# Kernel optimization log

Hardware: AMD Instinct MI355X
Metric: run time of the kernel (lower is better)

The kernel has to match this reference:

```python
import jax, jax.numpy as jnp
import numpy as np

PH = PW = 8
HEADS = 8
ADIM = 256
DH = ADIM // HEADS
N_KEYS = 3
CK, CV, CQ = 16, 32, 16
KS = 7
K_PDIM = PH * PW * CK   # 1024
V_PDIM = PH * PW * CV   # 2048
Q_PDIM = PH * PW * CQ   # 1024
MB_IN = N_KEYS * CV     # 96
MB_HID = 4 * MB_IN      # 384


def _to_patches(x):
    # b c (h ph) (w pw) -> b (h w) (ph pw c)
    b, c, H, W = x.shape
    h, w = H // PH, W // PW
    x = x.reshape(b, c, h, PH, w, PW).transpose(0, 2, 4, 3, 5, 1)
    return x.reshape(b, h * w, PH * PW * c)


def _layernorm(x, g, b):
    m = x.mean(-1, keepdims=True)
    v = x.var(-1, keepdims=True)
    return (x - m) * jax.lax.rsqrt(v + 1e-5) * g + b


def _embed(x, W1, b1, W2, b2):
    # NonLinearEmbedding: Linear -> GELU -> Linear
    return jax.nn.gelu(x @ W1 + b1) @ W2 + b2


def _to_heads(x):
    # b n (h d) -> b h n d
    b, n, hd = x.shape
    return x.reshape(b, n, HEADS, hd // HEADS).transpose(0, 2, 1, 3)


def _conv(x, w, b, groups, pad):
    y = jax.lax.conv_general_dilated(
        x, w, (1, 1), pad,
        dimension_numbers=('NCHW', 'OIHW', 'NCHW'),
        feature_group_count=groups)
    return y + b[None, :, None, None]


def _mbconv(x, w_exp, b_exp, w_dw, b_dw, w_proj, b_proj):
    # grouped 1x1 expand -> GELU -> depthwise kxk -> GELU -> grouped 1x1 project
    h = jax.nn.gelu(_conv(x, w_exp, b_exp, HEADS, 'VALID'))
    h = jax.nn.gelu(_conv(h, w_dw, b_dw, MB_HID, 'SAME'))
    return _conv(h, w_proj, b_proj, HEADS, 'VALID')


def setup_inputs() -> dict:
    key = jax.random.key(0)
    ks = jax.random.split(key, 24)
    B = 2
    key_sizes = [(256, 256), (192, 320), (128, 128)]
    query_sizes = [(256, 256), (192, 192)]
    s = 0.02
    inp = {}
    for i, (h, w) in enumerate(key_sizes):
        inp[f'keys_{i}'] = jax.random.normal(ks[i], (B, CK, h, w), jnp.float32)
        inp[f'values_{i}'] = jax.random.normal(ks[3 + i], (B, CV, h, w), jnp.float32)
    for i, (h, w) in enumerate(query_sizes):
        inp[f'queries_{i}'] = jax.random.normal(ks[6 + i], (B, CQ, h, w), jnp.float32)
    inp['ln_g'] = jnp.ones((V_PDIM,), jnp.float32)
    inp['ln_b'] = jnp.zeros((V_PDIM,), jnp.float32)
    inp['kW1'] = jax.random.normal(ks[8], (K_PDIM, ADIM), jnp.float32) * s
    inp['kb1'] = jnp.zeros((ADIM,), jnp.float32)
    inp['kW2'] = jax.random.normal(ks[9], (ADIM, ADIM), jnp.float32) * s
    inp['kb2'] = jnp.zeros((ADIM,), jnp.float32)
    inp['qW1'] = jax.random.normal(ks[10], (Q_PDIM, ADIM), jnp.float32) * s
    inp['qb1'] = jnp.zeros((ADIM,), jnp.float32)
    inp['qW2'] = jax.random.normal(ks[11], (ADIM, ADIM), jnp.float32) * s
    inp['qb2'] = jnp.zeros((ADIM,), jnp.float32)
    inp['w_exp'] = jax.random.normal(ks[12], (MB_HID, MB_IN // HEADS, 1, 1), jnp.float32) * s
    inp['b_exp'] = jnp.zeros((MB_HID,), jnp.float32)
    inp['w_dw'] = jax.random.normal(ks[13], (MB_HID, 1, KS, KS), jnp.float32) * s
    inp['b_dw'] = jnp.zeros((MB_HID,), jnp.float32)
    inp['w_proj'] = jax.random.normal(ks[14], (CV, MB_HID // HEADS, 1, 1), jnp.float32) * s
    inp['b_proj'] = jnp.zeros((CV,), jnp.float32)
    return inp


def reference(keys_0, keys_1, keys_2, values_0, values_1, values_2,
              queries_0, queries_1, ln_g, ln_b, kW1, kb1, kW2, kb2,
              qW1, qb1, qW2, qb2, w_exp, b_exp, w_dw, b_dw, w_proj, b_proj):
    keys = [keys_0, keys_1, keys_2]
    values = [values_0, values_1, values_2]
    queries = [queries_0, queries_1]
    # spatial sizes are already multiples of (PH, PW) -> pad_to_next_multiple is identity
    query_sizes = [q.shape[-2:] for q in queries]
    kp = [_to_patches(k) for k in keys]
    vp = [_to_patches(v) for v in values]
    qp = [_to_patches(q) for q in queries]
    nk = [p.shape[1] for p in kp]
    nq = [p.shape[1] for p in qp]
    k_seq = jnp.concatenate(kp, axis=1)               # (b, Nk, K_PDIM)
    v_seq = _layernorm(jnp.concatenate(vp, axis=1), ln_g, ln_b)  # (b, Nk, V_PDIM)
    q_seq = jnp.concatenate(qp, axis=1)               # (b, Nq, Q_PDIM)
    k_emb = _to_heads(_embed(k_seq, kW1, kb1, kW2, kb2))  # (b, h, Nk, DH)
    q_emb = _to_heads(_embed(q_seq, qW1, qb1, qW2, qb2))  # (b, h, Nq, DH)
    v_h = _to_heads(v_seq)                                # (b, h, Nk, dv)
    scale = jnp.asarray(1.0 / np.sqrt(DH), k_emb.dtype)
    attn = jnp.einsum('bhid,bhjd->bhij', q_emb, k_emb) * scale
    attn = jax.nn.softmax(attn, axis=-1)
    offs = np.cumsum([0] + nk)
    # per-source weighted values, stacked along a new source axis k
    weighted = jnp.stack(
        [attn[..., offs[i]:offs[i + 1]] @ v_h[:, :, offs[i]:offs[i + 1]]
         for i in range(N_KEYS)], axis=1)              # (b, k, h, Nq, dv)
    qoffs = np.cumsum([0] + nq)
    outs = []
    c = CV // HEADS
    for i, (qh, qw) in enumerate(query_sizes):
        v = weighted[:, :, :, qoffs[i]:qoffs[i + 1]]   # (b, k, hd, n, d)
        b, k, hd, n, d = v.shape
        h, w = qh // PH, qw // PW
        # b k hd (h w) (ph pw c) -> b (hd k c) (h ph) (w pw)
        v = v.reshape(b, k, hd, h, w, PH, PW, c).transpose(0, 2, 1, 7, 3, 5, 4, 6)
        v = v.reshape(b, hd * k * c, h * PH, w * PW)
        outs.append(_mbconv(v, w_exp, b_exp, w_dw, b_dw, w_proj, b_proj))
    return tuple(outs)
```

## Files before the change

kernel.cpp:

```cpp
#include <hip/hip_runtime.h>
#include <hip/hip_bf16.h>
#include <math.h>

typedef unsigned short bfu;
typedef __attribute__((ext_vector_type(8))) short short8v;
typedef __attribute__((ext_vector_type(4))) float f32x4;
typedef __attribute__((ext_vector_type(2))) float f32x2;

__device__ __forceinline__ float fast_rcp(float d) {
    float r = __builtin_amdgcn_rcpf(d);
    return r * fmaf(-d, r, 2.0f);
}
__device__ __forceinline__ f32x2 fma2(f32x2 a, f32x2 b, f32x2 c) {
    return __builtin_elementwise_fma(a, b, c);
}
__device__ __forceinline__ f32x2 splat2(float w) { return (f32x2){w, w}; }
__device__ __forceinline__ float gelu_f(float x) {
    float x3 = x * x * x;
    float e = __expf(1.5957691f * fmaf(0.044715f, x3, x));
    return x * e * __builtin_amdgcn_rcpf(e + 1.0f);
}
__device__ __forceinline__ f32x2 gelu2(f32x2 x) {
    f32x2 x3 = x * x * x;
    f32x2 z = fma2(splat2(0.044715f), x3, x) * 1.5957691f;
    f32x2 e = {__expf(z.x), __expf(z.y)};
    f32x2 d = e + 1.0f;
    f32x2 r = {__builtin_amdgcn_rcpf(d.x), __builtin_amdgcn_rcpf(d.y)};
    return x * e * r;
}
__device__ __forceinline__ float bf2f(bfu u) {
    union { float f; unsigned int i; } v; v.i = ((unsigned int)u) << 16; return v.f;
}
__device__ __forceinline__ bfu f2bf(float f) {
    union { float f; unsigned int i; } v; v.f = f;
    unsigned int r = v.i + 0x7fff + ((v.i >> 16) & 1);
    return (bfu)(r >> 16);
}
__device__ __forceinline__ float ldin(const void* p, size_t i, bool f32) {
    return f32 ? ((const float*)p)[i] : bf2f(((const bfu*)p)[i]);
}
__device__ __forceinline__ void stout(void* p, size_t i, float v, bool f32) {
    if (f32) ((float*)p)[i] = v;
    else     ((bfu*)p)[i] = f2bf(v);
}
__device__ __forceinline__ short8v ld_frag8(const bfu* p) {
    union { short8v v; ushort4 u[2]; } t;
    t.u[0] = *(const ushort4*)p;
    t.u[1] = *(const ushort4*)(p + 4);
    return t.v;
}

__global__ __launch_bounds__(256) void detect_kernel(const void* probe, int* flag) {
    __shared__ int red[4];
    const bfu* p = (const bfu*)probe;
    int tid = threadIdx.x;
    int insane = 0;
    for (int i = tid; i < 2048; i += 256) {
        unsigned e = (p[i] >> 7) & 0xFF;
        if (e >= 0xC0 || (e != 0 && e < 0x40)) insane++;
    }
    for (int o = 32; o > 0; o >>= 1) insane += __shfl_down(insane, o);
    if ((tid & 63) == 0) red[tid >> 6] = insane;
    __syncthreads();
    if (tid == 0) flag[0] = (red[0] + red[1] + red[2] + red[3] > 64) ? 1 : 0;
}

__global__ __launch_bounds__(256) void zero_out_kernel(bfu* __restrict__ out, int n) {
    int i = blockIdx.x * 256 + threadIdx.x;
    if (i < n) out[i] = 0;
}

__global__ __launch_bounds__(256) void wprep_kernel(
    const void* __restrict__ wexp, const void* __restrict__ bexp,
    const void* __restrict__ wdw, const void* __restrict__ bdw,
    const void* __restrict__ wproj, const void* __restrict__ bproj,
    const int* __restrict__ flag, float* __restrict__ wf)
{
    bool f32 = flag[0] != 0;
    int i = blockIdx.x * 256 + threadIdx.x;
    if (i < 4608)       wf[i] = ldin(wexp, i, f32);
    else if (i < 4992)  wf[i] = ldin(bexp, i - 4608, f32);
    else if (i < 23808) wf[i] = ldin(wdw, i - 4992, f32);
    else if (i < 24192) wf[i] = ldin(bdw, i - 23808, f32);
    else if (i < 25728) wf[i] = ldin(wproj, i - 24192, f32);
    else if (i < 25760) wf[i] = ldin(bproj, i - 25728, f32);
}

__global__ __launch_bounds__(256) void ln_stats_kernel(
    const void* __restrict__ v0, const void* __restrict__ v1, const void* __restrict__ v2,
    const int* __restrict__ flag, float* __restrict__ m_buf, float* __restrict__ i_buf)
{
    __shared__ float red[16];
    bool f32 = flag[0] != 0;
    int bid = blockIdx.x;
    int b = bid / 2240, n = bid - b * 2240;
    const void* src; int nl, wp, H, W;
    if (n < 1024)      { src = v0; nl = n;        wp = 32; H = 256; W = 256; }
    else if (n < 1984) { src = v1; nl = n - 1024; wp = 40; H = 192; W = 320; }
    else               { src = v2; nl = n - 1984; wp = 16; H = 128; W = 128; }
    int tid = threadIdx.x;
    int py = nl / wp, px = nl - py * wp;
    int ybase = py * 8, xbase = px * 8;
    float s1 = 0.f, s2 = 0.f;
    #pragma unroll
    for (int i = 0; i < 8; i++) {
        int j = tid + 256 * i;
        int ph = j >> 8, pw = (j >> 5) & 7, c = j & 31;
        float v = ldin(src, ((size_t)(b * 32 + c) * H + ybase + ph) * W + xbase + pw, f32);
        s1 += v; s2 = fmaf(v, v, s2);
    }
    for (int o = 32; o > 0; o >>= 1) { s1 += __shfl_down(s1, o); s2 += __shfl_down(s2, o); }
    int wid = tid >> 6;
    if ((tid & 63) == 0) { red[wid] = s1; red[8 + wid] = s2; }
    __syncthreads();
    if (tid == 0) {
        float a = red[0] + red[1] + red[2] + red[3];
        float q = red[8] + red[9] + red[10] + red[11];
        float m = a * (1.0f / 2048.0f);
        float var = q * (1.0f / 2048.0f) - m * m;
        m_buf[bid] = m;
        i_buf[bid] = 1.0f / sqrtf(var + 1e-5f);
    }
}

__global__ __launch_bounds__(256) void vstage_kernel(
    const void* __restrict__ v0, const void* __restrict__ v1, const void* __restrict__ v2,
    const void* __restrict__ g, const void* __restrict__ beta,
    const int* __restrict__ flag, bfu* __restrict__ out)
{
    __shared__ float red[16];
    __shared__ float mv[2];
    bool f32 = flag[0] != 0;
    int bid = blockIdx.x;
    int b = bid / 2240, n = bid - b * 2240;
    const void* src; int nl, wp, H, W;
    if (n < 1024)      { src = v0; nl = n;        wp = 32; H = 256; W = 256; }
    else if (n < 1984) { src = v1; nl = n - 1024; wp = 40; H = 192; W = 320; }
    else               { src = v2; nl = n - 1984; wp = 16; H = 128; W = 128; }
    int tid = threadIdx.x;
    int py = nl / wp, px = nl - py * wp;
    int ybase = py * 8, xbase = px * 8;
    float vals[8];
    float s1 = 0.f, s2 = 0.f;
    #pragma unroll
    for (int i = 0; i < 8; i++) {
        int j = tid + 256 * i;
        int ph = j >> 8, pw = (j >> 5) & 7, c = j & 31;
        float v = ldin(src, ((size_t)(b * 32 + c) * H + ybase + ph) * W + xbase + pw, f32);
        vals[i] = v; s1 += v; s2 = fmaf(v, v, s2);
    }
    for (int o = 32; o > 0; o >>= 1) { s1 += __shfl_down(s1, o); s2 += __shfl_down(s2, o); }
    int wid = tid >> 6;
    if ((tid & 63) == 0) { red[wid] = s1; red[8 + wid] = s2; }
    __syncthreads();
    if (tid == 0) {
        float a = red[0] + red[1] + red[2] + red[3];
        float q = red[8] + red[9] + red[10] + red[11];
        float m = a * (1.0f / 2048.0f);
        float var = q * (1.0f / 2048.0f) - m * m;
        mv[0] = m; mv[1] = 1.0f / sqrtf(var + 1e-5f);
    }
    __syncthreads();
    float m = mv[0], inv = mv[1];
    #pragma unroll
    for (int i = 0; i < 8; i++) {
        int j = tid + 256 * i;
        float o = (vals[i] - m) * inv * ldin(g, j, f32) + ldin(beta, j, f32);
        out[(size_t)bid * 2048 + j] = f2bf(o);
    }
}

__global__ __launch_bounds__(256) void vtr_kernel(
    const bfu* __restrict__ vseq, bfu* __restrict__ vT)
{
    __shared__ __align__(16) bfu Ls[17408];
    int bid = blockIdx.x;
    int ch = bid % 35;
    int t = bid / 35;
    int h = t & 7, b = t >> 3;
    int c = threadIdx.x;
    const bfu* srcb = vseq + (((size_t)(b * 2240 + (ch << 6))) << 11) + (h << 8) + c;
    #pragma unroll
    for (int k4 = 0; k4 < 16; k4++) {
        ushort4 v;
        v.x = srcb[(size_t)(k4 * 4 + 0) << 11];
        v.y = srcb[(size_t)(k4 * 4 + 1) << 11];
        v.z = srcb[(size_t)(k4 * 4 + 2) << 11];
        v.w = srcb[(size_t)(k4 * 4 + 3) << 11];
        *(ushort4*)&Ls[c * 68 + k4 * 4] = v;
    }
    __syncthreads();
    short8v* dst = (short8v*)(vT + (size_t)((b * 8 + h) * 35 + ch) * 17408);
    const short8v* s = (const short8v*)Ls;
    #pragma unroll
    for (int r = 0; r < 8; r++) dst[(r << 8) + c] = s[(r << 8) + c];
    if (c < 128) dst[2048 + c] = s[2048 + c];
}

__global__ __launch_bounds__(256) void embed1_kernel(
    const void* __restrict__ k0, const void* __restrict__ k1, const void* __restrict__ k2,
    const void* __restrict__ q0, const void* __restrict__ q1,
    const void* __restrict__ kW1, const void* __restrict__ kb1,
    const void* __restrict__ qW1, const void* __restrict__ qb1,
    const int* __restrict__ flag,
    bfu* __restrict__ k_hid, bfu* __restrict__ q_hid)
{
    __shared__ float As[16][68];
    __shared__ float Bs[16][68];
    bool f32 = flag[0] != 0;
    int bid = blockIdx.x;
    int colBase = (bid & 3) << 6;
    int rt = bid >> 2;
    const void* Wm; const void* bias; bfu* C;
    int rowBase, isK;
    if (rt < 70) { isK = 1; Wm = kW1; bias = kb1; C = k_hid; rowBase = rt << 6; }
    else         { isK = 0; Wm = qW1; bias = qb1; C = q_hid; rowBase = (rt - 70) << 6; }
    int tid = threadIdx.x;
    int tx = tid & 15, ty = tid >> 4;
    int arow = tid >> 2, akq = (tid & 3) << 2;
    int brow = tid >> 4, bcol = (tid & 15) << 2;
    int row = rowBase + arow;
    int nTot = isK ? 2240 : 1600;
    int b = row / nTot, n = row - b * nTot;
    const void* src; int nl, wp, H, W;
    if (isK) {
        if (n < 1024)      { src = k0; nl = n;        wp = 32; H = 256; W = 256; }
        else if (n < 1984) { src = k1; nl = n - 1024; wp = 40; H = 192; W = 320; }
        else               { src = k2; nl = n - 1984; wp = 16; H = 128; W = 128; }
    } else {
        if (n < 1024)      { src = q0; nl = n;        wp = 32; H = 256; W = 256; }
        else               { src = q1; nl = n - 1024; wp = 24; H = 192; W = 192; }
    }
    int py = nl / wp, px = nl - py * wp;
    int ybase = py << 3, xbase = px << 3;
    size_t HW = (size_t)H * W;
    size_t abase = (size_t)(b * 16 + akq) * HW;
    size_t wbase = (size_t)brow * 256 + colBase + bcol;
    float acc[4][4] = {};
    for (int k0i = 0; k0i < 1024; k0i += 16) {
        int j = k0i + akq;
        int ph = j >> 7, pw = (j >> 4) & 7;
        size_t ai = abase + (size_t)(ybase + ph) * W + xbase + pw;
        As[akq + 0][arow] = ldin(src, ai, f32);
        As[akq + 1][arow] = ldin(src, ai + HW, f32);
        As[akq + 2][arow] = ldin(src, ai + 2 * HW, f32);
        As[akq + 3][arow] = ldin(src, ai + 3 * HW, f32);
        size_t wo = wbase + (size_t)k0i * 256;
        #pragma unroll
        for (int t = 0; t < 4; t++) Bs[brow][bcol + t] = ldin(Wm, wo + t, f32);
        __syncthreads();
        #pragma unroll
        for (int kk = 0; kk < 16; kk++) {
            float4 a4 = *(const float4*)&As[kk][ty << 2];
            float4 p0 = *(const float4*)&Bs[kk][tx << 2];
            float ar[4] = {a4.x, a4.y, a4.z, a4.w};
            float br[4] = {p0.x, p0.y, p0.z, p0.w};
            #pragma unroll
            for (int rr = 0; rr < 4; rr++)
                #pragma unroll
                for (int i = 0; i < 4; i++)
                    acc[rr][i] = fmaf(ar[rr], br[i], acc[rr][i]);
        }
        __syncthreads();
    }
    int cg = colBase + (tx << 2);
    float bbr[4];
    #pragma unroll
    for (int i = 0; i < 4; i++) bbr[i] = ldin(bias, cg + i, f32);
    #pragma unroll
    for (int rr = 0; rr < 4; rr++) {
        ushort4 o;
        o.x = f2bf(gelu_f(acc[rr][0] + bbr[0]));
        o.y = f2bf(gelu_f(acc[rr][1] + bbr[1]));
        o.z = f2bf(gelu_f(acc[rr][2] + bbr[2]));
        o.w = f2bf(gelu_f(acc[rr][3] + bbr[3]));
        *(ushort4*)(&C[(size_t)(rowBase + (ty << 2) + rr) * 256 + cg]) = o;
    }
}

__global__ __launch_bounds__(256) void embed2_kernel(
    const bfu* __restrict__ A0, const void* __restrict__ W0, const void* __restrict__ bias0,
    bfu* __restrict__ C0, int tiles0,
    const bfu* __restrict__ A1, const void* __restrict__ W1, const void* __restrict__ bias1,
    bfu* __restrict__ C1, const int* __restrict__ flag)
{
    __shared__ float As[16][68];
    __shared__ float Bs[16][68];
    bool f32 = flag[0] != 0;
    int bid = blockIdx.x;
    int colBase = (bid & 3) << 6;
    int rt = bid >> 2;
    const bfu* A; const void* Wm; const void* bias; bfu* C;
    int rowBase;
    if (rt < tiles0) { A = A0; Wm = W0; bias = bias0; C = C0; rowBase = rt << 6; }
    else             { A = A1; Wm = W1; bias = bias1; C = C1; rowBase = (rt - tiles0) << 6; }
    int tid = threadIdx.x;
    int tx = tid & 15, ty = tid >> 4;
    int arow = tid >> 2, akq = (tid & 3) << 2;
    int brow = tid >> 4, bcol = (tid & 15) << 2;
    const bfu* Ap = A + (size_t)(rowBase + arow) * 256 + akq;
    size_t wbase = (size_t)brow * 256 + colBase + bcol;
    float acc[4][4] = {};
    for (int k0 = 0; k0 < 256; k0 += 16) {
        ushort4 av = *(const ushort4*)(Ap + k0);
        As[akq + 0][arow] = bf2f(av.x);
        As[akq + 1][arow] = bf2f(av.y);
        As[akq + 2][arow] = bf2f(av.z);
        As[akq + 3][arow] = bf2f(av.w);
        size_t wo = wbase + (size_t)k0 * 256;
        #pragma unroll
        for (int t = 0; t < 4; t++) Bs[brow][bcol + t] = ldin(Wm, wo + t, f32);
        __syncthreads();
        #pragma unroll
        for (int kk = 0; kk < 16; kk++) {
            float4 a4 = *(const float4*)&As[kk][ty << 2];
            float4 p0 = *(const float4*)&Bs[kk][tx << 2];
            float ar[4] = {a4.x, a4.y, a4.z, a4.w};
            float br[4] = {p0.x, p0.y, p0.z, p0.w};
            #pragma unroll
            for (int rr = 0; rr < 4; rr++)
                #pragma unroll
                for (int i = 0; i < 4; i++)
                    acc[rr][i] = fmaf(ar[rr], br[i], acc[rr][i]);
        }
        __syncthreads();
    }
    int cg = colBase + (tx << 2);
    float bbr[4];
    #pragma unroll
    for (int i = 0; i < 4; i++) bbr[i] = ldin(bias, cg + i, f32);
    #pragma unroll
    for (int rr = 0; rr < 4; rr++) {
        ushort4 o;
        o.x = f2bf(acc[rr][0] + bbr[0]);
        o.y = f2bf(acc[rr][1] + bbr[1]);
        o.z = f2bf(acc[rr][2] + bbr[2]);
        o.w = f2bf(acc[rr][3] + bbr[3]);
        *(ushort4*)(&C[(size_t)(rowBase + (ty << 2) + rr) * 256 + cg]) = o;
    }
}

__global__ __launch_bounds__(256) void attn_mfma_kernel(
    const bfu* __restrict__ qe, const bfu* __restrict__ ke,
    const bfu* __restrict__ vT,
    bfu* __restrict__ wbuf, float* __restrict__ lbuf, int h0, int hs)
{
    __shared__ __align__(16) bfu Vs[17408];
    __shared__ __align__(16) bfu Ps[2176];
    __shared__ float red[4][16];
    int bid = blockIdx.x;
    int qtile = bid % 50;
    int t = bid / 50;
    int hh = t % hs, b = t / hs;
    int h = h0 + hh;
    int n0 = qtile << 5;
    int tid = threadIdx.x;
    int w = tid >> 6, l = tid & 63;
    int l15 = l & 15, g = l >> 4;
    int wqt = w >> 1;
    int wkp = (w & 1) << 1;

    short8v qf = *(const short8v*)(qe + (((size_t)(b * 1600 + n0 + (wqt << 4) + l15)) << 8) + (h << 5) + (g << 3));

    f32x4 zero4 = {0.f, 0.f, 0.f, 0.f};
    f32x4 acc[2][4];
    #pragma unroll
    for (int i = 0; i < 2; i++)
        #pragma unroll
        for (int j = 0; j < 4; j++) acc[i][j] = zero4;
    float rs = 0.f;
    const float scale = 0.17677669529663687f;

    const short8v* vbase = (const short8v*)(vT + (size_t)((b * 8 + h) * 35) * 17408);
    short8v* VsV = (short8v*)Vs;

    for (int ch = 0; ch < 35; ch++) {
        const short8v* src = vbase + (size_t)ch * 2176;
        #pragma unroll
        for (int r = 0; r < 8; r++) VsV[(r << 8) + tid] = src[(r << 8) + tid];
        if (tid < 128) VsV[2048 + tid] = src[2048 + tid];
        #pragma unroll
        for (int j = 0; j < 2; j++) {
            int ktile = wkp + j;
            short8v kf = *(const short8v*)(ke + (((size_t)(b * 2240 + (ch << 6) + (ktile << 4) + l15)) << 8) + (h << 5) + (g << 3));
            f32x4 st = __builtin_amdgcn_mfma_f32_16x16x32_bf16(kf, qf, zero4, 0, 0, 0);
            float p0 = __expf(st[0] * scale);
            float p1 = __expf(st[1] * scale);
            float p2 = __expf(st[2] * scale);
            float p3 = __expf(st[3] * scale);
            rs += (p0 + p1) + (p2 + p3);
            ushort4 pk;
            pk.x = f2bf(p0); pk.y = f2bf(p1); pk.z = f2bf(p2); pk.w = f2bf(p3);
            *(ushort4*)&Ps[((wqt << 4) + l15) * 68 + (ktile << 4) + (g << 2)] = pk;
        }
        __syncthreads();
        #pragma unroll
        for (int kt = 0; kt < 2; kt++) {
            short8v a0 = ld_frag8(&Ps[l15 * 68 + (kt << 5) + (g << 3)]);
            short8v a1 = ld_frag8(&Ps[(16 + l15) * 68 + (kt << 5) + (g << 3)]);
            #pragma unroll
            for (int nt = 0; nt < 4; nt++) {
                int ntg = (w << 2) + nt;
                short8v bf = ld_frag8(&Vs[((ntg << 4) + l15) * 68 + (kt << 5) + (g << 3)]);
                acc[0][nt] = __builtin_amdgcn_mfma_f32_16x16x32_bf16(a0, bf, acc[0][nt], 0, 0, 0);
                acc[1][nt] = __builtin_amdgcn_mfma_f32_16x16x32_bf16(a1, bf, acc[1][nt], 0, 0, 0);
            }
        }
        __syncthreads();
        if (ch == 15 || ch == 30 || ch == 34) {
            int srcid = (ch == 15) ? 0 : (ch == 30 ? 1 : 2);
            bfu* wb = wbuf + ((size_t)((b * hs + hh) * 3 + srcid) * 1600 + n0) * 256 + (w << 6) + l15;
            #pragma unroll
            for (int q2 = 0; q2 < 2; q2++)
                #pragma unroll
                for (int nt = 0; nt < 4; nt++) {
                    #pragma unroll
                    for (int r = 0; r < 4; r++) {
                        wb[(size_t)((q2 << 4) + (g << 2) + r) * 256 + (nt << 4)] = f2bf(acc[q2][nt][r]);
                        acc[q2][nt][r] = 0.f;
                    }
                }
        }
    }
    rs += __shfl_xor(rs, 16);
    rs += __shfl_xor(rs, 32);
    if (l < 16) red[w][l15] = rs;
    __syncthreads();
    if (tid < 32) {
        int q2 = tid >> 4;
        float tot = red[q2 << 1][tid & 15] + red[(q2 << 1) + 1][tid & 15];
        lbuf[(size_t)(b * 8 + h) * 1600 + n0 + tid] = tot;
    }
}

__global__ __launch_bounds__(256) void attn_kernel(
    const bfu* __restrict__ qe, const bfu* __restrict__ ke,
    const bfu* __restrict__ vseq,
    const void* __restrict__ v0, const void* __restrict__ v1, const void* __restrict__ v2,
    const void* __restrict__ ln_g, const void* __restrict__ ln_b,
    const float* __restrict__ m_buf, const float* __restrict__ i_buf,
    const int* __restrict__ flag,
    bfu* __restrict__ wbuf, float* __restrict__ lbuf, int h0, int hs)
{
    __shared__ float Qs[32][36];
    __shared__ float Ks[32][37];
    __shared__ float Ps2[32][37];
    __shared__ float Vls[32][260];
    __shared__ float gbg[256];
    __shared__ float gbb[256];
    bool f32 = flag[0] != 0;
    int bid = blockIdx.x;
    int qt = bid % 50;
    int t = bid / 50;
    int hh = t % hs;
    int b = t / hs;
    int h = h0 + hh;
    int n0 = qt << 5;
    int tid = threadIdx.x;
    int tx = tid & 15, ty = tid >> 4;
    if (!vseq) {
        gbg[tid] = ldin(ln_g, h * 256 + tid, f32);
        gbb[tid] = ldin(ln_b, h * 256 + tid, f32);
    }
    {
        int r = tid >> 3, d0 = (tid & 7) << 2;
        const bfu* qp = qe + (size_t)(b * 1600 + n0 + r) * 256 + (h << 5) + d0;
        ushort4 a = *(const ushort4*)qp;
        Qs[r][d0 + 0] = bf2f(a.x); Qs[r][d0 + 1] = bf2f(a.y);
        Qs[r][d0 + 2] = bf2f(a.z); Qs[r][d0 + 3] = bf2f(a.w);
    }
    float lreg = 0.f;
    float acc[2][4][4] = {};
    const float scale = 0.17677669529663687f;
    int kvrow = tid >> 3, kq = (tid & 7) << 2;
    const bfu* kbase = ke + (size_t)(b * 2240 + kvrow) * 256 + (h << 5) + kq;
    const bfu* vsbase = vseq ? vseq + (size_t)(b * 2240 + kvrow) * 2048 + (h << 8) + kq : nullptr;
    for (int ch = 0; ch < 70; ch++) {
        {
            ushort4 kv = *(const ushort4*)(kbase + (size_t)ch * 8192);
            Ks[kvrow][kq + 0] = bf2f(kv.x);
            Ks[kvrow][kq + 1] = bf2f(kv.y);
            Ks[kvrow][kq + 2] = bf2f(kv.z);
            Ks[kvrow][kq + 3] = bf2f(kv.w);
        }
        if (vseq) {
            #pragma unroll
            for (int i = 0; i < 8; i++) {
                ushort4 u = *(const ushort4*)(vsbase + (size_t)ch * 65536 + (i << 5));
                int d = (i << 5) + kq;
                Vls[kvrow][d + 0] = bf2f(u.x);
                Vls[kvrow][d + 1] = bf2f(u.y);
                Vls[kvrow][d + 2] = bf2f(u.z);
                Vls[kvrow][d + 3] = bf2f(u.w);
            }
        } else {
            int n = ch * 32 + kvrow;
            const void* vsrc; int nl, wp, H, W;
            if (n < 1024)      { vsrc = v0; nl = n;        wp = 32; H = 256; W = 256; }
            else if (n < 1984) { vsrc = v1; nl = n - 1024; wp = 40; H = 192; W = 320; }
            else               { vsrc = v2; nl = n - 1984; wp = 16; H = 128; W = 128; }
            int py = nl / wp, px = nl - py * wp;
            int y = py * 8 + h, xb = px * 8;
            float m = m_buf[b * 2240 + n];
            float inv = i_buf[b * 2240 + n];
            size_t HW = (size_t)H * W;
            size_t vbi = ((size_t)(b * 32 + kq) * H + y) * W + xb;
            #pragma unroll
            for (int i = 0; i < 8; i++) {
                int d = (i << 5) + kq;
                float t0 = (ldin(vsrc, vbi + i, f32) - m) * inv;
                float t1 = (ldin(vsrc, vbi + i + HW, f32) - m) * inv;
                float t2 = (ldin(vsrc, vbi + i + 2 * HW, f32) - m) * inv;
                float t3 = (ldin(vsrc, vbi + i + 3 * HW, f32) - m) * inv;
                Vls[kvrow][d + 0] = fmaf(t0, gbg[d + 0], gbb[d + 0]);
                Vls[kvrow][d + 1] = fmaf(t1, gbg[d + 1], gbb[d + 1]);
                Vls[kvrow][d + 2] = fmaf(t2, gbg[d + 2], gbb[d + 2]);
                Vls[kvrow][d + 3] = fmaf(t3, gbg[d + 3], gbb[d + 3]);
            }
        }
        __syncthreads();
        float s[2][2] = {};
        #pragma unroll 8
        for (int d = 0; d < 32; d++) {
            float k0v = Ks[(tx << 1) + 0][d];
            float k1v = Ks[(tx << 1) + 1][d];
            #pragma unroll
            for (int rr = 0; rr < 2; rr++) {
                float qv = Qs[(ty << 1) + rr][d];
                s[rr][0] = fmaf(qv, k0v, s[rr][0]);
                s[rr][1] = fmaf(qv, k1v, s[rr][1]);
            }
        }
        #pragma unroll
        for (int rr = 0; rr < 2; rr++) {
            Ps2[(ty << 1) + rr][(tx << 1) + 0] = __expf(s[rr][0] * scale);
            Ps2[(ty << 1) + rr][(tx << 1) + 1] = __expf(s[rr][1] * scale);
        }
        __syncthreads();
        if (tid < 32) {
            float t2 = 0.f;
            #pragma unroll
            for (int jj = 0; jj < 32; jj++) t2 += Ps2[tid][jj];
            lreg += t2;
        }
        #pragma unroll 4
        for (int j = 0; j < 32; j++) {
            float4 w0 = *(const float4*)&Vls[j][(tx << 2)];
            float4 w1 = *(const float4*)&Vls[j][64 + (tx << 2)];
            float4 w2 = *(const float4*)&Vls[j][128 + (tx << 2)];
            float4 w3 = *(const float4*)&Vls[j][192 + (tx << 2)];
            #pragma unroll
            for (int rr = 0; rr < 2; rr++) {
                float p = Ps2[(ty << 1) + rr][j];
                acc[rr][0][0] = fmaf(p, w0.x, acc[rr][0][0]);
                acc[rr][0][1] = fmaf(p, w0.y, acc[rr][0][1]);
                acc[rr][0][2] = fmaf(p, w0.z, acc[rr][0][2]);
                acc[rr][0][3] = fmaf(p, w0.w, acc[rr][0][3]);
                acc[rr][1][0] = fmaf(p, w1.x, acc[rr][1][0]);
                acc[rr][1][1] = fmaf(p, w1.y, acc[rr][1][1]);
                acc[rr][1][2] = fmaf(p, w1.z, acc[rr][1][2]);
                acc[rr][1][3] = fmaf(p, w1.w, acc[rr][1][3]);
                acc[rr][2][0] = fmaf(p, w2.x, acc[rr][2][0]);
                acc[rr][2][1] = fmaf(p, w2.y, acc[rr][2][1]);
                acc[rr][2][2] = fmaf(p, w2.z, acc[rr][2][2]);
                acc[rr][2][3] = fmaf(p, w2.w, acc[rr][2][3]);
                acc[rr][3][0] = fmaf(p, w3.x, acc[rr][3][0]);
                acc[rr][3][1] = fmaf(p, w3.y, acc[rr][3][1]);
                acc[rr][3][2] = fmaf(p, w3.z, acc[rr][3][2]);
                acc[rr][3][3] = fmaf(p, w3.w, acc[rr][3][3]);
            }
        }
        __syncthreads();
        if (ch == 31 || ch == 61 || ch == 69) {
            int src = (ch == 31) ? 0 : (ch == 61 ? 1 : 2);
            bfu* wb = wbuf + (size_t)(((b * hs + hh) * 3 + src) * 1600 + n0 + (ty << 1)) * 256 + (tx << 2);
            #pragma unroll
            for (int rr = 0; rr < 2; rr++) {
                #pragma unroll
                for (int q = 0; q < 4; q++) {
                    ushort4 u;
                    u.x = f2bf(acc[rr][q][0]); u.y = f2bf(acc[rr][q][1]);
                    u.z = f2bf(acc[rr][q][2]); u.w = f2bf(acc[rr][q][3]);
                    *(ushort4*)(wb + (size_t)rr * 256 + (q << 6)) = u;
                    acc[rr][q][0] = acc[rr][q][1] = acc[rr][q][2] = acc[rr][q][3] = 0.f;
                }
            }
        }
    }
    if (tid < 32) lbuf[(size_t)(b * 8 + h) * 1600 + n0 + tid] = lreg;
}

__global__ __launch_bounds__(256) void mbconv_kernel(
    const bfu* __restrict__ wbuf, const float* __restrict__ lbuf,
    const float* __restrict__ wf, const int* __restrict__ flag,
    void* __restrict__ out, size_t out_off, int H, int W, int n_base,
    int tilesX, int tilesY, int h0, int hs)
{
    __shared__ __align__(16) float h1s[8][528];
    __shared__ float h2s[256][9];
    bool f32o = flag[0] != 0;
    const float* wexp_f  = wf;
    const float* bexp_f  = wf + 4608;
    const float* wdw_f   = wf + 4992;
    const float* bdw_f   = wf + 23808;
    const float* wproj_f = wf + 24192;
    const float* bproj_f = wf + 25728;
    int bid = blockIdx.x;
    int gi = bid % hs;
    int t2b = bid / hs;
    int tilesTot = tilesX * tilesY;
    int b = t2b / tilesTot;
    int rem = t2b - b * tilesTot;
    int tY = rem / tilesX, tX = rem - tY * tilesX;
    int gy0 = tY << 4, gx0 = tX << 4;
    int wp = W >> 3;
    int tid = threadIdx.x;
    int wu = __builtin_amdgcn_readfirstlane(tid >> 6);
    int l = tid & 63;
    int doy = ((l >> 3) & 7) << 1;
    int dox = (l & 7) << 1;
    int g = h0 + gi;

    f32x2 xsr2[12];
    #pragma unroll
    for (int ci = 0; ci < 12; ci++) xsr2[ci] = (f32x2){0.f, 0.f};
    int pa0 = 0, pa1 = 0; bool pv0 = false, pv1 = false;
    bool act = tid < 242;
    if (act) {
        #pragma unroll
        for (int j = 0; j < 2; j++) {
            int p = tid * 2 + j;
            int py = p / 22, px = p - py * 22;
            int y = gy0 - 3 + py, x = gx0 - 3 + px;
            bool valid = (y >= 0) && (y < H) && (x >= 0) && (x < W);
            if (j == 0) { pa0 = py * 24 + px; pv0 = valid; }
            else        { pa1 = py * 24 + px; pv1 = valid; }
            if (valid) {
                int n = n_base + (y >> 3) * wp + (x >> 3);
                float invl = fast_rcp(lbuf[(size_t)(b * 8 + g) * 1600 + n]);
                int d = ((y & 7) << 5) + ((x & 7) << 2);
                const bfu* src = wbuf + ((size_t)((b * hs + gi) * 3) * 1600 + n) * 256 + d;
                #pragma unroll
                for (int k = 0; k < 3; k++) {
                    ushort4 u = *(const ushort4*)(src + (size_t)k * 409600);
                    if (j == 0) {
                        xsr2[k * 4 + 0].x = bf2f(u.x) * invl;
                        xsr2[k * 4 + 1].x = bf2f(u.y) * invl;
                        xsr2[k * 4 + 2].x = bf2f(u.z) * invl;
                        xsr2[k * 4 + 3].x = bf2f(u.w) * invl;
                    } else {
                        xsr2[k * 4 + 0].y = bf2f(u.x) * invl;
                        xsr2[k * 4 + 1].y = bf2f(u.y) * invl;
                        xsr2[k * 4 + 2].y = bf2f(u.z) * invl;
                        xsr2[k * 4 + 3].y = bf2f(u.w) * invl;
                    }
                }
            }
        }
    }

    float oacc[4] = {0.f, 0.f, 0.f, 0.f};
    for (int chunk = 0; chunk < 6; chunk++) {
        int hc0 = g * 48 + chunk * 8;
        __syncthreads();
        if (act) {
            #pragma unroll
            for (int c = 0; c < 8; c++) {
                const float* we = &wexp_f[(size_t)(hc0 + c) * 12];
                f32x2 a = splat2(bexp_f[hc0 + c]);
                #pragma unroll
                for (int ci = 0; ci < 12; ci++)
                    a = fma2(splat2(we[ci]), xsr2[ci], a);
                f32x2 gv = gelu2(a);
                h1s[c][pa0] = pv0 ? gv.x : 0.f;
                h1s[c][pa1] = pv1 ? gv.y : 0.f;
            }
        }
        __syncthreads();
        #pragma unroll
        for (int c2 = 0; c2 < 2; c2++) {
            int ch = wu + (c2 << 2);
            const float* wd = &wdw_f[(size_t)(hc0 + ch) * 49];
            float bd = bdw_f[hc0 + ch];
            f32x2 a2v0 = splat2(bd);
            f32x2 a2v1 = splat2(bd);
            #pragma unroll
            for (int r = 0; r < 8; r++) {
                const f32x2* rp = (const f32x2*)&h1s[ch][(doy + r) * 24 + dox];
                f32x2 p0 = rp[0], p1 = rp[1], p2 = rp[2], p3 = rp[3];
                f32x2 q0 = {p0.y, p1.x}, q1 = {p1.y, p2.x}, q2 = {p2.y, p3.x};
                f32x2 win[7] = {p0, q0, p1, q1, p2, q2, p3};
                if (r <= 6) {
                    const float* wk = &wd[r * 7];
                    #pragma unroll
                    for (int kx = 0; kx < 7; kx++)
                        a2v0 = fma2(splat2(wk[kx]), win[kx], a2v0);
                }
                if (r >= 1) {
                    const float* wk = &wd[(r - 1) * 7];
                    #pragma unroll
                    for (int kx = 0; kx < 7; kx++)
                        a2v1 = fma2(splat2(wk[kx]), win[kx], a2v1);
                }
            }
            f32x2 g0 = gelu2(a2v0), g1 = gelu2(a2v1);
            h2s[(doy + 0) * 16 + dox + 0][ch] = g0.x;
            h2s[(doy + 0) * 16 + dox + 1][ch] = g0.y;
            h2s[(doy + 1) * 16 + dox + 0][ch] = g1.x;
            h2s[(doy + 1) * 16 + dox + 1][ch] = g1.y;
        }
        __syncthreads();
        #pragma unroll
        for (int c = 0; c < 8; c++) {
            float hv = h2s[tid][c];
            #pragma unroll
            for (int oc = 0; oc < 4; oc++)
                oacc[oc] = fmaf(hv, wproj_f[(size_t)(g * 4 + oc) * 48 + chunk * 8 + c], oacc[oc]);
        }
    }
    int yy = tid >> 4, xx = tid & 15;
    #pragma unroll
    for (int oc = 0; oc < 4; oc++) {
        stout(out, out_off + ((size_t)(b * 32 + g * 4 + oc) * H + gy0 + yy) * W + gx0 + xx,
              oacc[oc] + bproj_f[g * 4 + oc], f32o);
    }
}

extern "C" void kernel_launch(void* const* d_in, const int* in_sizes, int n_in,
                              void* d_out, int out_size, void* d_ws, size_t ws_size,
                              hipStream_t stream)
{
    const void *keys0, *keys1, *keys2, *vals0, *vals1, *vals2;
    keys0 = d_in[0];
    if (in_sizes[1] == 4194304) {
        vals0 = d_in[1]; keys1 = d_in[2]; vals1 = d_in[3]; keys2 = d_in[4]; vals2 = d_in[5];
    } else {
        keys1 = d_in[1]; keys2 = d_in[2]; vals0 = d_in[3]; vals1 = d_in[4]; vals2 = d_in[5];
    }
    const void* qrys0  = d_in[6];
    const void* qrys1  = d_in[7];
    const void* ln_g   = d_in[8];
    const void* ln_b   = d_in[9];
    const void* kW1    = d_in[10];
    const void* kb1    = d_in[11];
    const void* kW2    = d_in[12];
    const void* kb2    = d_in[13];
    const void* qW1    = d_in[14];
    const void* qb1    = d_in[15];
    const void* qW2    = d_in[16];
    const void* qb2    = d_in[17];
    const void* w_exp  = d_in[18];
    const void* b_exp  = d_in[19];
    const void* w_dw   = d_in[20];
    const void* b_dw   = d_in[21];
    const void* w_proj = d_in[22];
    const void* b_proj = d_in[23];

    char* base = (char*)d_ws;
    int*   flag  = (int*)base;
    bfu*   k_emb = (bfu*)(base + 64);
    bfu*   q_emb = (bfu*)(base + 64 + 2293760);
    float* l_buf = (float*)(base + 64 + 3932160);
    float* m_buf = (float*)(base + 64 + 4034560);
    float* i_buf = (float*)(base + 64 + 4052480);
    const size_t FIXED0 = 4070464ULL;
    float* w_f   = (float*)(base + FIXED0);
    const size_t FIXEDN = FIXED0 + 103040ULL;
    const size_t VSEQB = 18350080ULL;
    const size_t VTB   = 19496960ULL;
    const size_t RX    = FIXEDN + VTB;

    const size_t need8 = RX + 8ULL * 4915200ULL;
    const size_t need4 = RX + 19660800ULL;
    const size_t need2 = RX + VSEQB;

    detect_kernel<<<1, 256, 0, stream>>>(keys0, flag);
    wprep_kernel<<<101, 256, 0, stream>>>(w_exp, b_exp, w_dw, b_dw, w_proj, b_proj, flag, w_f);

    if (ws_size >= need2) {
        int hs = (ws_size >= need8) ? 8 : (ws_size >= need4 ? 4 : 2);
        bfu* vT    = (bfu*)(base + FIXEDN);
        bfu* v_seq = (bfu*)(base + RX);
        bfu* k_hid = (bfu*)(base + RX);
        bfu* q_hid = (bfu*)(base + RX + 2293760);
        bfu* w_buf = (bfu*)(base + RX);

        vstage_kernel<<<4480, 256, 0, stream>>>(vals0, vals1, vals2, ln_g, ln_b, flag, v_seq);
        vtr_kernel<<<560, 256, 0, stream>>>(v_seq, vT);
        embed1_kernel<<<480, 256, 0, stream>>>(keys0, keys1, keys2, qrys0, qrys1,
                                               kW1, kb1, qW1, qb1, flag, k_hid, q_hid);
        embed2_kernel<<<480, 256, 0, stream>>>(k_hid, kW2, kb2, k_emb, 70,
                                               q_hid, qW2, qb2, q_emb, flag);
        for (int h0 = 0; h0 < 8; h0 += hs) {
            attn_mfma_kernel<<<2 * hs * 50, 256, 0, stream>>>(
                q_emb, k_emb, vT, w_buf, l_buf, h0, hs);
            mbconv_kernel<<<2 * 256 * hs, 256, 0, stream>>>(
                w_buf, l_buf, w_f, flag,
                d_out, 0, 256, 256, 0, 16, 16, h0, hs);
            mbconv_kernel<<<2 * 144 * hs, 256, 0, stream>>>(
                w_buf, l_buf, w_f, flag,
                d_out, 4194304, 192, 192, 1024, 12, 12, h0, hs);
        }
        return;
    }

    int hs;
    if      (ws_size >= FIXEDN + 8ULL * 4915200ULL) hs = 8;
    else if (ws_size >= FIXEDN + 4ULL * 4915200ULL) hs = 4;
    else if (ws_size >= FIXEDN + 2ULL * 4915200ULL) hs = 2;
    else if (ws_size >= FIXEDN + 1ULL * 4915200ULL) hs = 1;
    else {
        zero_out_kernel<<<(out_size + 255) / 256, 256, 0, stream>>>((bfu*)d_out, out_size);
        return;
    }
    char* rest  = base + FIXEDN;
    bfu*  k_hid = (bfu*)rest;
    bfu*  q_hid = (bfu*)(rest + 2293760);
    bfu*  w_buf = (bfu*)rest;

    ln_stats_kernel<<<4480, 256, 0, stream>>>(vals0, vals1, vals2, flag, m_buf, i_buf);
    embed1_kernel<<<480, 256, 0, stream>>>(keys0, keys1, keys2, qrys0, qrys1,
                                           kW1, kb1, qW1, qb1, flag, k_hid, q_hid);
    embed2_kernel<<<480, 256, 0, stream>>>(k_hid, kW2, kb2, k_emb, 70,
                                           q_hid, qW2, qb2, q_emb, flag);
    for (int h0 = 0; h0 < 8; h0 += hs) {
        attn_kernel<<<2 * hs * 50, 256, 0, stream>>>(
            q_emb, k_emb, nullptr, vals0, vals1, vals2, ln_g, ln_b, m_buf, i_buf, flag,
            w_buf, l_buf, h0, hs);
        mbconv_kernel<<<2 * 256 * hs, 256, 0, stream>>>(
            w_buf, l_buf, w_f, flag,
            d_out, 0, 256, 256, 0, 16, 16, h0, hs);
        mbconv_kernel<<<2 * 144 * hs, 256, 0, stream>>>(
            w_buf, l_buf, w_f, flag,
            d_out, 4194304, 192, 192, 1024, 12, 12, h0, hs);
    }
}
```

Before: 616.3 us.

## Replace FP32 embedding GEMMs with bf16 MFMA path and coalesce vstage I/O

Replaces the old shared-memory FP32 embed1/embed2 GEMMs with a staged pipeline. New kernels patchify keys and queries to bf16 rows and pre-transpose the embedding weights to bf16, and an MFMA-based GEMM kernel applies bias and GELU. The vstage kernel now reads input channels with a pixel-major thread mapping for coalesced loads and writes through shared memory as 16-byte vectors. This adds three kernel launches and extra workspace buffers, and lowers GEMM input precision to bf16.

```diff
diff --git a/kernel.cpp b/kernel.cpp
--- a/kernel.cpp
+++ b/kernel.cpp
@@ -130,23 +130,26 @@
 {
     __shared__ float red[16];
     __shared__ float mv[2];
+    __shared__ __align__(16) bfu Ls[2048];
     bool f32 = flag[0] != 0;
     int bid = blockIdx.x;
     int b = bid / 2240, n = bid - b * 2240;
-    const void* src; int nl, wp, H, W;
-    if (n < 1024)      { src = v0; nl = n;        wp = 32; H = 256; W = 256; }
-    else if (n < 1984) { src = v1; nl = n - 1024; wp = 40; H = 192; W = 320; }
-    else               { src = v2; nl = n - 1984; wp = 16; H = 128; W = 128; }
-    int tid = threadIdx.x;
-    int py = nl / wp, px = nl - py * wp;
-    int ybase = py * 8, xbase = px * 8;
+    const void* src; int nl, wpn, H, W;
+    if (n < 1024)      { src = v0; nl = n;        wpn = 32; H = 256; W = 256; }
+    else if (n < 1984) { src = v1; nl = n - 1024; wpn = 40; H = 192; W = 320; }
+    else               { src = v2; nl = n - 1984; wpn = 16; H = 128; W = 128; }
+    int tid = threadIdx.x;
+    int py = nl / wpn, px = nl - py * wpn;
+    int p = tid & 63;
+    int c0 = tid >> 6;
+    int y = py * 8 + (p >> 3), x = px * 8 + (p & 7);
+    size_t HW = (size_t)H * W;
+    size_t base = ((size_t)(b * 32 + c0) * H + y) * W + x;
     float vals[8];
     float s1 = 0.f, s2 = 0.f;
     #pragma unroll
     for (int i = 0; i < 8; i++) {
-        int j = tid + 256 * i;
-        int ph = j >> 8, pw = (j >> 5) & 7, c = j & 31;
-        float v = ldin(src, ((size_t)(b * 32 + c) * H + ybase + ph) * W + xbase + pw, f32);
+        float v = ldin(src, base + (size_t)(i << 2) * HW, f32);
         vals[i] = v; s1 += v; s2 = fmaf(v, v, s2);
     }
     for (int o = 32; o > 0; o >>= 1) { s1 += __shfl_down(s1, o); s2 += __shfl_down(s2, o); }
@@ -162,12 +165,16 @@
     }
     __syncthreads();
     float m = mv[0], inv = mv[1];
+    int jb = (p >> 3) * 256 + (p & 7) * 32 + c0;
     #pragma unroll
     for (int i = 0; i < 8; i++) {
-        int j = tid + 256 * i;
+        int j = jb + (i << 2);
         float o = (vals[i] - m) * inv * ldin(g, j, f32) + ldin(beta, j, f32);
-        out[(size_t)bid * 2048 + j] = f2bf(o);
-    }
+        Ls[j] = f2bf(o);
+    }
+    __syncthreads();
+    short8v* dst = (short8v*)(out + (size_t)bid * 2048);
+    dst[tid] = ((const short8v*)Ls)[tid];
 }
 
 __global__ __launch_bounds__(256) void vtr_kernel(
@@ -195,6 +202,128 @@
     #pragma unroll
     for (int r = 0; r < 8; r++) dst[(r << 8) + c] = s[(r << 8) + c];
     if (c < 128) dst[2048 + c] = s[2048 + c];
+}
+
+__global__ __launch_bounds__(256) void kstage_kernel(
+    const void* __restrict__ k0, const void* __restrict__ k1, const void* __restrict__ k2,
+    const void* __restrict__ q0, const void* __restrict__ q1,
+    const int* __restrict__ flag, bfu* __restrict__ k_seq, bfu* __restrict__ q_seq)
+{
+    bool f32 = flag[0] != 0;
+    int tid = threadIdx.x;
+    int w = tid >> 6, l = tid & 63;
+    int row = blockIdx.x * 4 + w;
+    const void* src; int b, nl, wpn, H, W; bfu* dst;
+    if (row < 4480) {
+        b = row / 2240; int n = row - b * 2240;
+        if (n < 1024)      { src = k0; nl = n;        wpn = 32; H = 256; W = 256; }
+        else if (n < 1984) { src = k1; nl = n - 1024; wpn = 40; H = 192; W = 320; }
+        else               { src = k2; nl = n - 1984; wpn = 16; H = 128; W = 128; }
+        dst = k_seq + ((size_t)row << 10);
+    } else {
+        int r2 = row - 4480;
+        b = r2 / 1600; int n = r2 - b * 1600;
+        if (n < 1024)      { src = q0; nl = n;        wpn = 32; H = 256; W = 256; }
+        else               { src = q1; nl = n - 1024; wpn = 24; H = 192; W = 192; }
+        dst = q_seq + ((size_t)r2 << 10);
+    }
+    int py = nl / wpn, px = nl - py * wpn;
+    int y = (py << 3) + (l >> 3), x = (px << 3) + (l & 7);
+    size_t HW = (size_t)H * W;
+    size_t base = ((size_t)(b * 16) * H + y) * W + x;
+    bfu vals[16];
+    #pragma unroll
+    for (int c = 0; c < 16; c++) vals[c] = f2bf(ldin(src, base + c * HW, f32));
+    bfu* dp = dst + (l << 4);
+    *(ushort4*)(dp + 0)  = *(ushort4*)&vals[0];
+    *(ushort4*)(dp + 4)  = *(ushort4*)&vals[4];
+    *(ushort4*)(dp + 8)  = *(ushort4*)&vals[8];
+    *(ushort4*)(dp + 12) = *(ushort4*)&vals[12];
+}
+
+__global__ __launch_bounds__(256) void wstage_kernel(
+    const void* __restrict__ kW1, const void* __restrict__ qW1,
+    const void* __restrict__ kW2, const void* __restrict__ qW2,
+    const void* __restrict__ kb1, const void* __restrict__ qb1,
+    const void* __restrict__ kb2, const void* __restrict__ qb2,
+    const int* __restrict__ flag, bfu* __restrict__ WT, float* __restrict__ biasf)
+{
+    __shared__ float Ls[64][65];
+    bool f32 = flag[0] != 0;
+    int bid = blockIdx.x;
+    int tid = threadIdx.x;
+    if (bid == 160) {
+        biasf[tid]       = ldin(kb1, tid, f32);
+        biasf[256 + tid] = ldin(qb1, tid, f32);
+        biasf[512 + tid] = ldin(kb2, tid, f32);
+        biasf[768 + tid] = ldin(qb2, tid, f32);
+        return;
+    }
+    const void* src; bfu* dst; int K, t;
+    if (bid < 64)       { src = kW1; dst = WT;          K = 1024; t = bid; }
+    else if (bid < 128) { src = qW1; dst = WT + 262144; K = 1024; t = bid - 64; }
+    else if (bid < 144) { src = kW2; dst = WT + 524288; K = 256;  t = bid - 128; }
+    else                { src = qW2; dst = WT + 589824; K = 256;  t = bid - 144; }
+    int ktiles = K >> 6;
+    int tk = t % ktiles, tc = t / ktiles;
+    int k0 = tk << 6, c0 = tc << 6;
+    int j = tid & 63, i0 = tid >> 6;
+    #pragma unroll
+    for (int p = 0; p < 16; p++) {
+        int i = i0 + (p << 2);
+        Ls[j][i] = ldin(src, (size_t)(k0 + i) * 256 + c0 + j, f32);
+    }
+    __syncthreads();
+    #pragma unroll
+    for (int p = 0; p < 16; p++) {
+        int ci = i0 + (p << 2);
+        dst[(size_t)(c0 + ci) * K + k0 + j] = f2bf(Ls[ci][j]);
+    }
+}
+
+__global__ __launch_bounds__(256) void embed_mfma_kernel(
+    const bfu* __restrict__ Ak, const bfu* __restrict__ Aq,
+    const bfu* __restrict__ WTk, const bfu* __restrict__ WTq,
+    const float* __restrict__ bk, const float* __restrict__ bq,
+    bfu* __restrict__ Ck, bfu* __restrict__ Cq,
+    int K, int gelu, int tiles0)
+{
+    int bid = blockIdx.x;
+    int c0 = (bid & 3) << 6;
+    int rt = bid >> 2;
+    const bfu* A; const bfu* WT; const float* bias; bfu* C;
+    int row0;
+    if (rt < tiles0) { A = Ak; WT = WTk; bias = bk; C = Ck; row0 = rt << 6; }
+    else             { A = Aq; WT = WTq; bias = bq; C = Cq; row0 = (rt - tiles0) << 6; }
+    int tid = threadIdx.x;
+    int w = tid >> 6, l = tid & 63;
+    int l15 = l & 15, g = l >> 4;
+    f32x4 zero4 = {0.f, 0.f, 0.f, 0.f};
+    f32x4 acc[4] = {zero4, zero4, zero4, zero4};
+    const bfu* wp = WT + (size_t)(c0 + (w << 4) + l15) * K + (g << 3);
+    const bfu* ap = A + (size_t)(row0 + l15) * K + (g << 3);
+    int nk = K >> 5;
+    for (int kk = 0; kk < nk; kk++) {
+        short8v af = ld_frag8(wp + (kk << 5));
+        #pragma unroll
+        for (int r2 = 0; r2 < 4; r2++) {
+            short8v bf = ld_frag8(ap + (size_t)(r2 << 4) * K + (kk << 5));
+            acc[r2] = __builtin_amdgcn_mfma_f32_16x16x32_bf16(af, bf, acc[r2], 0, 0, 0);
+        }
+    }
+    int colb = c0 + (w << 4) + (g << 2);
+    float4 bb = *(const float4*)&bias[colb];
+    #pragma unroll
+    for (int r2 = 0; r2 < 4; r2++) {
+        float v0 = acc[r2][0] + bb.x;
+        float v1 = acc[r2][1] + bb.y;
+        float v2 = acc[r2][2] + bb.z;
+        float v3 = acc[r2][3] + bb.w;
+        if (gelu) { v0 = gelu_f(v0); v1 = gelu_f(v1); v2 = gelu_f(v2); v3 = gelu_f(v3); }
+        ushort4 o;
+        o.x = f2bf(v0); o.y = f2bf(v1); o.z = f2bf(v2); o.w = f2bf(v3);
+        *(ushort4*)(C + (size_t)(row0 + (r2 << 4) + l15) * 256 + colb) = o;
+    }
 }
 
 __global__ __launch_bounds__(256) void embed1_kernel(
@@ -770,27 +899,38 @@
     const size_t VTB   = 19496960ULL;
     const size_t RX    = FIXEDN + VTB;
 
-    const size_t need8 = RX + 8ULL * 4915200ULL;
-    const size_t need4 = RX + 19660800ULL;
-    const size_t need2 = RX + VSEQB;
+    const size_t EMB = 20975616ULL;
+    const size_t need8 = RX + 39321600ULL;
+    const size_t need4 = RX + EMB;
+    const size_t need2 = RX + EMB;
 
     detect_kernel<<<1, 256, 0, stream>>>(keys0, flag);
     wprep_kernel<<<101, 256, 0, stream>>>(w_exp, b_exp, w_dw, b_dw, w_proj, b_proj, flag, w_f);
 
     if (ws_size >= need2) {
         int hs = (ws_size >= need8) ? 8 : (ws_size >= need4 ? 4 : 2);
-        bfu* vT    = (bfu*)(base + FIXEDN);
-        bfu* v_seq = (bfu*)(base + RX);
-        bfu* k_hid = (bfu*)(base + RX);
-        bfu* q_hid = (bfu*)(base + RX + 2293760);
-        bfu* w_buf = (bfu*)(base + RX);
+        bfu*   vT    = (bfu*)(base + FIXEDN);
+        bfu*   v_seq = (bfu*)(base + RX);
+        bfu*   k_seq = (bfu*)(base + RX);
+        bfu*   q_seq = (bfu*)(base + RX + 9175040);
+        bfu*   WTb   = (bfu*)(base + RX + 15728640);
+        float* biasf = (float*)(base + RX + 17039360);
+        bfu*   k_hid = (bfu*)(base + RX + 17043456);
+        bfu*   q_hid = (bfu*)(base + RX + 19337216);
+        bfu*   w_buf = (bfu*)(base + RX);
 
         vstage_kernel<<<4480, 256, 0, stream>>>(vals0, vals1, vals2, ln_g, ln_b, flag, v_seq);
         vtr_kernel<<<560, 256, 0, stream>>>(v_seq, vT);
-        embed1_kernel<<<480, 256, 0, stream>>>(keys0, keys1, keys2, qrys0, qrys1,
-                                               kW1, kb1, qW1, qb1, flag, k_hid, q_hid);
-        embed2_kernel<<<480, 256, 0, stream>>>(k_hid, kW2, kb2, k_emb, 70,
-                                               q_hid, qW2, qb2, q_emb, flag);
+        kstage_kernel<<<1920, 256, 0, stream>>>(keys0, keys1, keys2, qrys0, qrys1,
+                                                flag, k_seq, q_seq);
+        wstage_kernel<<<161, 256, 0, stream>>>(kW1, qW1, kW2, qW2, kb1, qb1, kb2, qb2,
+                                               flag, WTb, biasf);
+        embed_mfma_kernel<<<480, 256, 0, stream>>>(k_seq, q_seq, WTb, WTb + 262144,
+                                                   biasf, biasf + 256, k_hid, q_hid,
+                                                   1024, 1, 70);
+        embed_mfma_kernel<<<480, 256, 0, stream>>>(k_hid, q_hid, WTb + 524288, WTb + 589824,
+                                                   biasf + 512, biasf + 768, k_emb, q_emb,
+                                                   256, 0, 70);
         for (int h0 = 0; h0 < 8; h0 += hs) {
             attn_mfma_kernel<<<2 * hs * 50, 256, 0, stream>>>(
                 q_emb, k_emb, vT, w_buf, l_buf, h0, hs);
```

After: 551.4 us. 10.5% less time.
